# Kernel tuning notes

Hardware: AMD Instinct MI355X
Metric: run time of the kernel (lower is better)

The kernel has to match this reference:

```python
import jax, jax.numpy as jnp
import numpy as np

B, W, F = 32, 128, 64      # batch, window (node feat dim), n_features (nodes)
H, D = 2, 128              # num_heads, out_window_size
NEG_SLOPE = 0.2


def setup_inputs() -> dict:
    key = jax.random.key(0)
    k1, k2, k3, k4, k5 = jax.random.split(key, 5)
    s = 1.0 / np.sqrt(W)
    return {
        "x": jax.random.normal(k1, (B, W, F), dtype=jnp.float32),
        "Wl": jax.random.normal(k2, (W, H * D), dtype=jnp.float32) * s,   # fc_src
        "Wr": jax.random.normal(k3, (W, H * D), dtype=jnp.float32) * s,   # fc_dst
        "attn_a": jax.random.normal(k4, (H, D), dtype=jnp.float32) * s,   # GATv2 attn vector
        "bias": jax.random.normal(k5, (H * D,), dtype=jnp.float32) * 0.01,
    }


def reference(x, Wl, Wr, attn_a, bias):
    """Dense batched GATv2 over a complete graph (with self loops) per batch.

    Matches DGL GATv2Conv (share_weights=False, bias=True, eval mode so
    feat_drop/attn_drop are identity), followed by mean over heads and the
    [B,F,D] -> [B,D,F] transpose of DGLFeatureGAT.forward.
    """
    # node features: x [B, W, F] -> [B, F, W]
    xn = jnp.swapaxes(x, 1, 2)
    el = jnp.einsum('bnw,whd->bnhd', xn, Wl.reshape(W, H, D))  # fc_src(h)
    er = jnp.einsum('bnw,whd->bnhd', xn, Wr.reshape(W, H, D))  # fc_dst(h)
    # edge (src=j -> dst=i): e_ij = a_h . LeakyReLU(el_j + er_i)
    pair = el[:, None, :, :, :] + er[:, :, None, :, :]          # [B, i, j, H, D]
    e = jnp.einsum('bijhd,hd->bhij', jax.nn.leaky_relu(pair, NEG_SLOPE), attn_a)
    # softmax over incoming edges (src j) per dst i
    alpha = jax.nn.softmax(e, axis=-1)                          # [B, H, i, j]
    rst = jnp.einsum('bhij,bjhd->bihd', alpha, el)              # aggregate fc_src feats
    rst = rst + bias.reshape(1, 1, H, D)
    out = rst.mean(axis=2)                                      # mean over heads -> [B, F, D]
    return jnp.swapaxes(out, 1, 2)                              # [B, D, F]
```

## Files before the change

kernel.cpp:

```cpp
#include <hip/hip_runtime.h>
#include <hip/hip_bf16.h>


constexpr int kB = 32, kW = 128, kF = 64, kH = 2, kD = 128, kHD = 256;
constexpr float kNeg = 0.2f;

__device__ __forceinline__ float lrelu(float v) { return fmaxf(v, kNeg * v); }

__global__ __launch_bounds__(512) void gat_proj(
    const float* __restrict__ x, const float* __restrict__ Wl,
    const float* __restrict__ Wr, float* __restrict__ elw,
    float* __restrict__ erw) {
  __shared__ float xw[kW][kF + 4];
  const int b = blockIdx.x >> 3;
  const int c0 = (blockIdx.x & 7) << 5;
  const int t = threadIdx.x;

  const float* xb = x + b * (kW * kF);
#pragma unroll
  for (int k = 0; k < 16; ++k) {
    const int idx = t + (k << 9);
    xw[idx >> 6][idx & 63] = xb[idx];
  }
  __syncthreads();

  const int c = c0 + (t & 31);
  const int n0 = (t >> 5) << 2;
  float accl[4] = {0.f, 0.f, 0.f, 0.f};
  float accr[4] = {0.f, 0.f, 0.f, 0.f};
  const float* wlp = Wl + c;
  const float* wrp = Wr + c;

#pragma unroll 8
  for (int w = 0; w < kW; ++w) {
    const float wl = wlp[w * kHD];
    const float wr = wrp[w * kHD];
    const float4 xa = *(const float4*)&xw[w][n0];
    accl[0] = fmaf(xa.x, wl, accl[0]); accr[0] = fmaf(xa.x, wr, accr[0]);
    accl[1] = fmaf(xa.y, wl, accl[1]); accr[1] = fmaf(xa.y, wr, accr[1]);
    accl[2] = fmaf(xa.z, wl, accl[2]); accr[2] = fmaf(xa.z, wr, accr[2]);
    accl[3] = fmaf(xa.w, wl, accl[3]); accr[3] = fmaf(xa.w, wr, accr[3]);
  }

  const int base = (b * kF + n0) * kHD + c;
#pragma unroll
  for (int k = 0; k < 4; ++k) {
    elw[base + k * kHD] = accl[k];
    erw[base + k * kHD] = accr[k];
  }
}

__global__ __launch_bounds__(512) void gat_attn(
    const float* __restrict__ elw, const float* __restrict__ erw,
    const float* __restrict__ attn_a, const float* __restrict__ bias,
    float* __restrict__ out) {
  __shared__ float el[kH][kF][kD + 4];
  __shared__ float sAT[kH][kF][8];
  __shared__ float pbuf[4][kH][8][kD + 4];

  const int b = blockIdx.x >> 3;
  const int i0 = (blockIdx.x & 7) << 3;
  const int t = threadIdx.x;

  {
    const float* elb = elw + b * (kF * kHD);
#pragma unroll
    for (int k = 0; k < 8; ++k) {
      const int s = t + (k << 9);
      const int h = s >> 11;
      const int n = (s >> 5) & 63;
      const int dv = (s & 31) << 2;
      *(float4*)&el[h][n][dv] = *(const float4*)&elb[n * kHD + h * kD + dv];
    }
  }
  __syncthreads();

  {
    const int q = t & 15;
    const int jh = (t >> 4) & 1;
    const int i = (t >> 5) & 7;
    const int h = t >> 8;
    const int j0 = q + (jh << 5);
    const int j1 = j0 + 16;
    const float* erp = erw + (b * kF + i0 + i) * kHD + h * kD;
    const float* avp = attn_a + h * kD;
    float e0 = 0.f, e1 = 0.f;
#pragma unroll
    for (int dv = 0; dv < kD; dv += 4) {
      const float4 rv = *(const float4*)&erp[dv];
      const float4 a4 = *(const float4*)&avp[dv];
      const float4 p0 = *(const float4*)&el[h][j0][dv];
      const float4 p1 = *(const float4*)&el[h][j1][dv];
      e0 = fmaf(lrelu(p0.x + rv.x), a4.x, e0);
      e0 = fmaf(lrelu(p0.y + rv.y), a4.y, e0);
      e0 = fmaf(lrelu(p0.z + rv.z), a4.z, e0);
      e0 = fmaf(lrelu(p0.w + rv.w), a4.w, e0);
      e1 = fmaf(lrelu(p1.x + rv.x), a4.x, e1);
      e1 = fmaf(lrelu(p1.y + rv.y), a4.y, e1);
      e1 = fmaf(lrelu(p1.z + rv.z), a4.z, e1);
      e1 = fmaf(lrelu(p1.w + rv.w), a4.w, e1);
    }
    float m = fmaxf(e0, e1);
#pragma unroll
    for (int off = 1; off < 32; off <<= 1) m = fmaxf(m, __shfl_xor(m, off));
    const float x0 = __expf(e0 - m);
    const float x1 = __expf(e1 - m);
    float s = x0 + x1;
#pragma unroll
    for (int off = 1; off < 32; off <<= 1) s += __shfl_xor(s, off);
    const float inv = 1.f / s;
    sAT[h][j0][i] = x0 * inv;
    sAT[h][j1][i] = x1 * inv;
  }
  __syncthreads();

  {
    const int dq = t & 31;
    const int ip = (t >> 5) & 1;
    const int jq = (t >> 6) & 3;
    const int h = t >> 8;
    float acc[4][4] = {};
    const int jbase = jq << 4;
#pragma unroll
    for (int jj = 0; jj < 16; ++jj) {
      const int j = jbase + jj;
      const float4 al = *(const float4*)&sAT[h][j][ip << 2];
      const float4 ev = *(const float4*)&el[h][j][dq << 2];
      acc[0][0] = fmaf(al.x, ev.x, acc[0][0]);
      acc[0][1] = fmaf(al.x, ev.y, acc[0][1]);
      acc[0][2] = fmaf(al.x, ev.z, acc[0][2]);
      acc[0][3] = fmaf(al.x, ev.w, acc[0][3]);
      acc[1][0] = fmaf(al.y, ev.x, acc[1][0]);
      acc[1][1] = fmaf(al.y, ev.y, acc[1][1]);
      acc[1][2] = fmaf(al.y, ev.z, acc[1][2]);
      acc[1][3] = fmaf(al.y, ev.w, acc[1][3]);
      acc[2][0] = fmaf(al.z, ev.x, acc[2][0]);
      acc[2][1] = fmaf(al.z, ev.y, acc[2][1]);
      acc[2][2] = fmaf(al.z, ev.z, acc[2][2]);
      acc[2][3] = fmaf(al.z, ev.w, acc[2][3]);
      acc[3][0] = fmaf(al.w, ev.x, acc[3][0]);
      acc[3][1] = fmaf(al.w, ev.y, acc[3][1]);
      acc[3][2] = fmaf(al.w, ev.z, acc[3][2]);
      acc[3][3] = fmaf(al.w, ev.w, acc[3][3]);
    }
#pragma unroll
    for (int ii = 0; ii < 4; ++ii) {
      float4 v;
      v.x = acc[ii][0]; v.y = acc[ii][1]; v.z = acc[ii][2]; v.w = acc[ii][3];
      *(float4*)&pbuf[jq][h][(ip << 2) + ii][dq << 2] = v;
    }
  }
  __syncthreads();

  {
    const int i = t & 7;
    const int d = (t >> 3) << 1;
    float o0 = 0.f, o1 = 0.f;
#pragma unroll
    for (int jq = 0; jq < 4; ++jq) {
#pragma unroll
      for (int h = 0; h < 2; ++h) {
        const float2 v = *(const float2*)&pbuf[jq][h][i][d];
        o0 += v.x;
        o1 += v.y;
      }
    }
    const float b0 = bias[d] + bias[kD + d];
    const float b1 = bias[d + 1] + bias[kD + d + 1];
    float* ob = out + b * (kD * kF) + i0 + i;
    ob[d * kF] = 0.5f * (o0 + b0);
    ob[(d + 1) * kF] = 0.5f * (o1 + b1);
  }
}

extern "C" void kernel_launch(void* const* d_in, const int* in_sizes, int n_in,
                              void* d_out, int out_size, void* d_ws,
                              size_t ws_size, hipStream_t stream) {
  (void)in_sizes; (void)n_in; (void)ws_size; (void)out_size;
  const float* x = (const float*)d_in[0];
  const float* Wl = (const float*)d_in[1];
  const float* Wr = (const float*)d_in[2];
  const float* attn_a = (const float*)d_in[3];
  const float* bias = (const float*)d_in[4];
  float* out = (float*)d_out;

  float* elw = (float*)d_ws;
  float* erw = elw + (size_t)kB * kF * kHD;

  gat_proj<<<dim3(kB * 8), dim3(512), 0, stream>>>(x, Wl, Wr, elw, erw);
  gat_attn<<<dim3(kB * 8), dim3(512), 0, stream>>>(elw, erw, attn_a, bias, out);
}
```

Before: 24.85 us.

## Fuse projection and attention into one kernel, recomputing el per block

Merges the projection and attention kernels into a single kernel. Each block now recomputes the full el projection for its batch in shared memory, plus er for its own 8 destination nodes, instead of round-tripping through a global workspace. This removes one launch and the global write/read of el/er, at the cost of 8x redundant el projection work across the blocks of a batch. Shared memory is reused between the x tile and the partial-sum buffer, and the output store is vectorized as float2 along F.

```diff
diff --git a/kernel.cpp b/kernel.cpp
--- a/kernel.cpp
+++ b/kernel.cpp
@@ -7,89 +7,94 @@
 
 __device__ __forceinline__ float lrelu(float v) { return fmaxf(v, kNeg * v); }
 
-__global__ __launch_bounds__(512) void gat_proj(
+#define XW(w, n) u[(w) * 68 + (n)]
+#define PBUF(jp, h, i, d) u[(((jp) * 2 + (h)) * 8 + (i)) * 132 + (d)]
+
+__global__ __launch_bounds__(512) void gat_fused(
     const float* __restrict__ x, const float* __restrict__ Wl,
-    const float* __restrict__ Wr, float* __restrict__ elw,
-    float* __restrict__ erw) {
-  __shared__ float xw[kW][kF + 4];
+    const float* __restrict__ Wr, const float* __restrict__ attn_a,
+    const float* __restrict__ bias, float* __restrict__ out) {
+  __shared__ float el[kH][kF][kD + 4];
+  __shared__ float er[kH][8][kD + 4];
+  __shared__ float sAT[kH][kF][8];
+  __shared__ float u[8704];
+
   const int b = blockIdx.x >> 3;
-  const int c0 = (blockIdx.x & 7) << 5;
+  const int i0 = (blockIdx.x & 7) << 3;
   const int t = threadIdx.x;
 
   const float* xb = x + b * (kW * kF);
 #pragma unroll
   for (int k = 0; k < 16; ++k) {
     const int idx = t + (k << 9);
-    xw[idx >> 6][idx & 63] = xb[idx];
-  }
-  __syncthreads();
-
-  const int c = c0 + (t & 31);
-  const int n0 = (t >> 5) << 2;
-  float accl[4] = {0.f, 0.f, 0.f, 0.f};
-  float accr[4] = {0.f, 0.f, 0.f, 0.f};
-  const float* wlp = Wl + c;
-  const float* wrp = Wr + c;
-
-#pragma unroll 8
-  for (int w = 0; w < kW; ++w) {
-    const float wl = wlp[w * kHD];
-    const float wr = wrp[w * kHD];
-    const float4 xa = *(const float4*)&xw[w][n0];
-    accl[0] = fmaf(xa.x, wl, accl[0]); accr[0] = fmaf(xa.x, wr, accr[0]);
-    accl[1] = fmaf(xa.y, wl, accl[1]); accr[1] = fmaf(xa.y, wr, accr[1]);
-    accl[2] = fmaf(xa.z, wl, accl[2]); accr[2] = fmaf(xa.z, wr, accr[2]);
-    accl[3] = fmaf(xa.w, wl, accl[3]); accr[3] = fmaf(xa.w, wr, accr[3]);
-  }
-
-  const int base = (b * kF + n0) * kHD + c;
-#pragma unroll
-  for (int k = 0; k < 4; ++k) {
-    elw[base + k * kHD] = accl[k];
-    erw[base + k * kHD] = accr[k];
-  }
-}
-
-__global__ __launch_bounds__(512) void gat_attn(
-    const float* __restrict__ elw, const float* __restrict__ erw,
-    const float* __restrict__ attn_a, const float* __restrict__ bias,
-    float* __restrict__ out) {
-  __shared__ float el[kH][kF][kD + 4];
-  __shared__ float sAT[kH][kF][8];
-  __shared__ float pbuf[4][kH][8][kD + 4];
-
-  const int b = blockIdx.x >> 3;
-  const int i0 = (blockIdx.x & 7) << 3;
-  const int t = threadIdx.x;
-
-  {
-    const float* elb = elw + b * (kF * kHD);
-#pragma unroll
-    for (int k = 0; k < 8; ++k) {
-      const int s = t + (k << 9);
-      const int h = s >> 11;
-      const int n = (s >> 5) & 63;
-      const int dv = (s & 31) << 2;
-      *(float4*)&el[h][n][dv] = *(const float4*)&elb[n * kHD + h * kD + dv];
-    }
+    XW(idx >> 6, idx & 63) = xb[idx];
   }
   __syncthreads();
 
   {
-    const int q = t & 15;
-    const int jh = (t >> 4) & 1;
+    const int dg = t & 31;
+    const int j0 = (t >> 5) << 2;
+    const int c = dg << 2;
+    float a0[4][4] = {};
+    float a1[4][4] = {};
+    const float* w0p = Wl + c;
+    const float* w1p = Wl + kD + c;
+#pragma unroll 4
+    for (int w = 0; w < kW; ++w) {
+      const float4 w0 = *(const float4*)&w0p[w * kHD];
+      const float4 w1 = *(const float4*)&w1p[w * kHD];
+      const float4 xv = *(const float4*)&XW(w, j0);
+      const float xa[4] = {xv.x, xv.y, xv.z, xv.w};
+      const float wa0[4] = {w0.x, w0.y, w0.z, w0.w};
+      const float wa1[4] = {w1.x, w1.y, w1.z, w1.w};
+#pragma unroll
+      for (int jj = 0; jj < 4; ++jj)
+#pragma unroll
+        for (int cc = 0; cc < 4; ++cc) {
+          a0[jj][cc] = fmaf(xa[jj], wa0[cc], a0[jj][cc]);
+          a1[jj][cc] = fmaf(xa[jj], wa1[cc], a1[jj][cc]);
+        }
+    }
+#pragma unroll
+    for (int jj = 0; jj < 4; ++jj) {
+      *(float4*)&el[0][j0 + jj][c] =
+          make_float4(a0[jj][0], a0[jj][1], a0[jj][2], a0[jj][3]);
+      *(float4*)&el[1][j0 + jj][c] =
+          make_float4(a1[jj][0], a1[jj][1], a1[jj][2], a1[jj][3]);
+    }
+  }
+
+  {
+    const int i = t >> 6;
+    const int c = (t & 63) << 2;
+    const int n = i0 + i;
+    float a[4] = {};
+    const float* wrp = Wr + c;
+#pragma unroll 4
+    for (int w = 0; w < kW; ++w) {
+      const float xs = XW(w, n);
+      const float4 w4 = *(const float4*)&wrp[w * kHD];
+      a[0] = fmaf(xs, w4.x, a[0]);
+      a[1] = fmaf(xs, w4.y, a[1]);
+      a[2] = fmaf(xs, w4.z, a[2]);
+      a[3] = fmaf(xs, w4.w, a[3]);
+    }
+    *(float4*)&er[c >> 7][i][c & 127] = make_float4(a[0], a[1], a[2], a[3]);
+  }
+  __syncthreads();
+
+  {
+    const int jl = t & 31;
     const int i = (t >> 5) & 7;
     const int h = t >> 8;
-    const int j0 = q + (jh << 5);
-    const int j1 = j0 + 16;
-    const float* erp = erw + (b * kF + i0 + i) * kHD + h * kD;
+    const int j1 = jl + 32;
     const float* avp = attn_a + h * kD;
     float e0 = 0.f, e1 = 0.f;
 #pragma unroll
     for (int dv = 0; dv < kD; dv += 4) {
-      const float4 rv = *(const float4*)&erp[dv];
       const float4 a4 = *(const float4*)&avp[dv];
-      const float4 p0 = *(const float4*)&el[h][j0][dv];
+      const float4 rv = *(const float4*)&er[h][i][dv];
+      const float4 p0 = *(const float4*)&el[h][jl][dv];
       const float4 p1 = *(const float4*)&el[h][j1][dv];
       e0 = fmaf(lrelu(p0.x + rv.x), a4.x, e0);
       e0 = fmaf(lrelu(p0.y + rv.y), a4.y, e0);
@@ -109,23 +114,24 @@
 #pragma unroll
     for (int off = 1; off < 32; off <<= 1) s += __shfl_xor(s, off);
     const float inv = 1.f / s;
-    sAT[h][j0][i] = x0 * inv;
+    sAT[h][jl][i] = x0 * inv;
     sAT[h][j1][i] = x1 * inv;
   }
   __syncthreads();
 
   {
-    const int dq = t & 31;
-    const int ip = (t >> 5) & 1;
-    const int jq = (t >> 6) & 3;
-    const int h = t >> 8;
+    const int ip = t & 1;
+    const int dg = (t >> 1) & 31;
+    const int h = (t >> 6) & 1;
+    const int jp = t >> 7;
+    const int d0 = dg << 2;
+    const int ib = ip << 2;
     float acc[4][4] = {};
-    const int jbase = jq << 4;
 #pragma unroll
     for (int jj = 0; jj < 16; ++jj) {
-      const int j = jbase + jj;
-      const float4 al = *(const float4*)&sAT[h][j][ip << 2];
-      const float4 ev = *(const float4*)&el[h][j][dq << 2];
+      const int j = (jp << 4) + jj;
+      const float4 al = *(const float4*)&sAT[h][j][ib];
+      const float4 ev = *(const float4*)&el[h][j][d0];
       acc[0][0] = fmaf(al.x, ev.x, acc[0][0]);
       acc[0][1] = fmaf(al.x, ev.y, acc[0][1]);
       acc[0][2] = fmaf(al.x, ev.z, acc[0][2]);
@@ -145,38 +151,36 @@
     }
 #pragma unroll
     for (int ii = 0; ii < 4; ++ii) {
-      float4 v;
-      v.x = acc[ii][0]; v.y = acc[ii][1]; v.z = acc[ii][2]; v.w = acc[ii][3];
-      *(float4*)&pbuf[jq][h][(ip << 2) + ii][dq << 2] = v;
+      *(float4*)&PBUF(jp, h, ib + ii, d0) =
+          make_float4(acc[ii][0], acc[ii][1], acc[ii][2], acc[ii][3]);
     }
   }
   __syncthreads();
 
   {
-    const int i = t & 7;
-    const int d = (t >> 3) << 1;
-    float o0 = 0.f, o1 = 0.f;
+    const int ipr = t & 3;
+    const int d = t >> 2;
+    float s0 = 0.f, s1 = 0.f;
 #pragma unroll
-    for (int jq = 0; jq < 4; ++jq) {
+    for (int jp = 0; jp < 4; ++jp)
 #pragma unroll
       for (int h = 0; h < 2; ++h) {
-        const float2 v = *(const float2*)&pbuf[jq][h][i][d];
-        o0 += v.x;
-        o1 += v.y;
+        const float* p = &PBUF(jp, h, ipr << 1, d);
+        s0 += p[0];
+        s1 += p[132];
       }
-    }
-    const float b0 = bias[d] + bias[kD + d];
-    const float b1 = bias[d + 1] + bias[kD + d + 1];
-    float* ob = out + b * (kD * kF) + i0 + i;
-    ob[d * kF] = 0.5f * (o0 + b0);
-    ob[(d + 1) * kF] = 0.5f * (o1 + b1);
+    const float bs = 0.5f * (bias[d] + bias[kD + d]);
+    float2 v;
+    v.x = 0.5f * s0 + bs;
+    v.y = 0.5f * s1 + bs;
+    *(float2*)&out[b * (kD * kF) + d * kF + i0 + (ipr << 1)] = v;
   }
 }
 
 extern "C" void kernel_launch(void* const* d_in, const int* in_sizes, int n_in,
                               void* d_out, int out_size, void* d_ws,
                               size_t ws_size, hipStream_t stream) {
-  (void)in_sizes; (void)n_in; (void)ws_size; (void)out_size;
+  (void)in_sizes; (void)n_in; (void)d_ws; (void)ws_size; (void)out_size;
   const float* x = (const float*)d_in[0];
   const float* Wl = (const float*)d_in[1];
   const float* Wr = (const float*)d_in[2];
@@ -184,9 +188,6 @@
   const float* bias = (const float*)d_in[4];
   float* out = (float*)d_out;
 
-  float* elw = (float*)d_ws;
-  float* erw = elw + (size_t)kB * kF * kHD;
-
-  gat_proj<<<dim3(kB * 8), dim3(512), 0, stream>>>(x, Wl, Wr, elw, erw);
-  gat_attn<<<dim3(kB * 8), dim3(512), 0, stream>>>(elw, erw, attn_a, bias, out);
+  gat_fused<<<dim3(kB * 8), dim3(512), 0, stream>>>(x, Wl, Wr, attn_a, bias,
+                                                    out);
 }
```

After: 32.85 us. 1.32x slower.

## Double threads per block and split per-thread work in GAT kernels

Applied to the files above, without the earlier changes.

Both kernels move from 512 to 1024 threads per block, and each thread does half the work. In the projection each thread now computes 2 nodes instead of 4. In the attention score phase the D reduction is split across two thread halves and combined with a cross-lane shuffle, and each thread also uses two accumulators. The aggregation now handles 2 rows per thread, and the final reduce writes one output per thread. The goal is more parallelism and latency hiding with only 256 blocks on the device, at the cost of extra shuffles and heavier per-block register and LDS pressure.

```diff
diff --git a/kernel.cpp b/kernel.cpp
--- a/kernel.cpp
+++ b/kernel.cpp
@@ -7,7 +7,7 @@
 
 __device__ __forceinline__ float lrelu(float v) { return fmaxf(v, kNeg * v); }
 
-__global__ __launch_bounds__(512) void gat_proj(
+__global__ __launch_bounds__(1024) void gat_proj(
     const float* __restrict__ x, const float* __restrict__ Wl,
     const float* __restrict__ Wr, float* __restrict__ elw,
     float* __restrict__ erw) {
@@ -18,16 +18,15 @@
 
   const float* xb = x + b * (kW * kF);
 #pragma unroll
-  for (int k = 0; k < 16; ++k) {
-    const int idx = t + (k << 9);
+  for (int k = 0; k < 8; ++k) {
+    const int idx = t + (k << 10);
     xw[idx >> 6][idx & 63] = xb[idx];
   }
   __syncthreads();
 
   const int c = c0 + (t & 31);
-  const int n0 = (t >> 5) << 2;
-  float accl[4] = {0.f, 0.f, 0.f, 0.f};
-  float accr[4] = {0.f, 0.f, 0.f, 0.f};
+  const int n0 = (t >> 5) << 1;
+  float l0 = 0.f, l1 = 0.f, r0 = 0.f, r1 = 0.f;
   const float* wlp = Wl + c;
   const float* wrp = Wr + c;
 
@@ -35,22 +34,21 @@
   for (int w = 0; w < kW; ++w) {
     const float wl = wlp[w * kHD];
     const float wr = wrp[w * kHD];
-    const float4 xa = *(const float4*)&xw[w][n0];
-    accl[0] = fmaf(xa.x, wl, accl[0]); accr[0] = fmaf(xa.x, wr, accr[0]);
-    accl[1] = fmaf(xa.y, wl, accl[1]); accr[1] = fmaf(xa.y, wr, accr[1]);
-    accl[2] = fmaf(xa.z, wl, accl[2]); accr[2] = fmaf(xa.z, wr, accr[2]);
-    accl[3] = fmaf(xa.w, wl, accl[3]); accr[3] = fmaf(xa.w, wr, accr[3]);
+    const float2 xa = *(const float2*)&xw[w][n0];
+    l0 = fmaf(xa.x, wl, l0);
+    r0 = fmaf(xa.x, wr, r0);
+    l1 = fmaf(xa.y, wl, l1);
+    r1 = fmaf(xa.y, wr, r1);
   }
 
   const int base = (b * kF + n0) * kHD + c;
-#pragma unroll
-  for (int k = 0; k < 4; ++k) {
-    elw[base + k * kHD] = accl[k];
-    erw[base + k * kHD] = accr[k];
-  }
+  elw[base] = l0;
+  elw[base + kHD] = l1;
+  erw[base] = r0;
+  erw[base + kHD] = r1;
 }
 
-__global__ __launch_bounds__(512) void gat_attn(
+__global__ __launch_bounds__(1024) void gat_attn(
     const float* __restrict__ elw, const float* __restrict__ erw,
     const float* __restrict__ attn_a, const float* __restrict__ bias,
     float* __restrict__ out) {
@@ -65,8 +63,8 @@
   {
     const float* elb = elw + b * (kF * kHD);
 #pragma unroll
-    for (int k = 0; k < 8; ++k) {
-      const int s = t + (k << 9);
+    for (int k = 0; k < 4; ++k) {
+      const int s = t + (k << 10);
       const int h = s >> 11;
       const int n = (s >> 5) & 63;
       const int dv = (s & 31) << 2;
@@ -78,28 +76,46 @@
   {
     const int q = t & 15;
     const int jh = (t >> 4) & 1;
-    const int i = (t >> 5) & 7;
-    const int h = t >> 8;
+    const int dh = (t >> 5) & 1;
+    const int i = (t >> 6) & 7;
+    const int h = t >> 9;
     const int j0 = q + (jh << 5);
     const int j1 = j0 + 16;
     const float* erp = erw + (b * kF + i0 + i) * kHD + h * kD;
     const float* avp = attn_a + h * kD;
-    float e0 = 0.f, e1 = 0.f;
+    const int dvb = dh << 6;
+    float e0a = 0.f, e0b = 0.f, e1a = 0.f, e1b = 0.f;
 #pragma unroll
-    for (int dv = 0; dv < kD; dv += 4) {
+    for (int k = 0; k < 16; ++k) {
+      const int dv = dvb + (k << 2);
+      const float4 a4 = *(const float4*)&avp[dv];
       const float4 rv = *(const float4*)&erp[dv];
-      const float4 a4 = *(const float4*)&avp[dv];
       const float4 p0 = *(const float4*)&el[h][j0][dv];
       const float4 p1 = *(const float4*)&el[h][j1][dv];
-      e0 = fmaf(lrelu(p0.x + rv.x), a4.x, e0);
-      e0 = fmaf(lrelu(p0.y + rv.y), a4.y, e0);
-      e0 = fmaf(lrelu(p0.z + rv.z), a4.z, e0);
-      e0 = fmaf(lrelu(p0.w + rv.w), a4.w, e0);
-      e1 = fmaf(lrelu(p1.x + rv.x), a4.x, e1);
-      e1 = fmaf(lrelu(p1.y + rv.y), a4.y, e1);
-      e1 = fmaf(lrelu(p1.z + rv.z), a4.z, e1);
-      e1 = fmaf(lrelu(p1.w + rv.w), a4.w, e1);
+      if (k & 1) {
+        e0b = fmaf(lrelu(p0.x + rv.x), a4.x, e0b);
+        e0b = fmaf(lrelu(p0.y + rv.y), a4.y, e0b);
+        e0b = fmaf(lrelu(p0.z + rv.z), a4.z, e0b);
+        e0b = fmaf(lrelu(p0.w + rv.w), a4.w, e0b);
+        e1b = fmaf(lrelu(p1.x + rv.x), a4.x, e1b);
+        e1b = fmaf(lrelu(p1.y + rv.y), a4.y, e1b);
+        e1b = fmaf(lrelu(p1.z + rv.z), a4.z, e1b);
+        e1b = fmaf(lrelu(p1.w + rv.w), a4.w, e1b);
+      } else {
+        e0a = fmaf(lrelu(p0.x + rv.x), a4.x, e0a);
+        e0a = fmaf(lrelu(p0.y + rv.y), a4.y, e0a);
+        e0a = fmaf(lrelu(p0.z + rv.z), a4.z, e0a);
+        e0a = fmaf(lrelu(p0.w + rv.w), a4.w, e0a);
+        e1a = fmaf(lrelu(p1.x + rv.x), a4.x, e1a);
+        e1a = fmaf(lrelu(p1.y + rv.y), a4.y, e1a);
+        e1a = fmaf(lrelu(p1.z + rv.z), a4.z, e1a);
+        e1a = fmaf(lrelu(p1.w + rv.w), a4.w, e1a);
+      }
     }
+    float e0 = e0a + e0b;
+    float e1 = e1a + e1b;
+    e0 += __shfl_xor(e0, 32);
+    e1 += __shfl_xor(e1, 32);
     float m = fmaxf(e0, e1);
 #pragma unroll
     for (int off = 1; off < 32; off <<= 1) m = fmaxf(m, __shfl_xor(m, off));
@@ -116,16 +132,17 @@
 
   {
     const int dq = t & 31;
-    const int ip = (t >> 5) & 1;
-    const int jq = (t >> 6) & 3;
-    const int h = t >> 8;
-    float acc[4][4] = {};
-    const int jbase = jq << 4;
+    const int jq = (t >> 5) & 3;
+    const int isel = (t >> 7) & 3;
+    const int h = t >> 9;
+    const int d0 = dq << 2;
+    const int i2 = isel << 1;
+    float acc[2][4] = {};
 #pragma unroll
     for (int jj = 0; jj < 16; ++jj) {
-      const int j = jbase + jj;
-      const float4 al = *(const float4*)&sAT[h][j][ip << 2];
-      const float4 ev = *(const float4*)&el[h][j][dq << 2];
+      const int j = (jq << 4) + jj;
+      const float2 al = *(const float2*)&sAT[h][j][i2];
+      const float4 ev = *(const float4*)&el[h][j][d0];
       acc[0][0] = fmaf(al.x, ev.x, acc[0][0]);
       acc[0][1] = fmaf(al.x, ev.y, acc[0][1]);
       acc[0][2] = fmaf(al.x, ev.z, acc[0][2]);
@@ -134,42 +151,24 @@
       acc[1][1] = fmaf(al.y, ev.y, acc[1][1]);
       acc[1][2] = fmaf(al.y, ev.z, acc[1][2]);
       acc[1][3] = fmaf(al.y, ev.w, acc[1][3]);
-      acc[2][0] = fmaf(al.z, ev.x, acc[2][0]);
-      acc[2][1] = fmaf(al.z, ev.y, acc[2][1]);
-      acc[2][2] = fmaf(al.z, ev.z, acc[2][2]);
-      acc[2][3] = fmaf(al.z, ev.w, acc[2][3]);
-      acc[3][0] = fmaf(al.w, ev.x, acc[3][0]);
-      acc[3][1] = fmaf(al.w, ev.y, acc[3][1]);
-      acc[3][2] = fmaf(al.w, ev.z, acc[3][2]);
-      acc[3][3] = fmaf(al.w, ev.w, acc[3][3]);
     }
-#pragma unroll
-    for (int ii = 0; ii < 4; ++ii) {
-      float4 v;
-      v.x = acc[ii][0]; v.y = acc[ii][1]; v.z = acc[ii][2]; v.w = acc[ii][3];
-      *(float4*)&pbuf[jq][h][(ip << 2) + ii][dq << 2] = v;
-    }
+    *(float4*)&pbuf[jq][h][i2][d0] =
+        make_float4(acc[0][0], acc[0][1], acc[0][2], acc[0][3]);
+    *(float4*)&pbuf[jq][h][i2 + 1][d0] =
+        make_float4(acc[1][0], acc[1][1], acc[1][2], acc[1][3]);
   }
   __syncthreads();
 
   {
     const int i = t & 7;
-    const int d = (t >> 3) << 1;
-    float o0 = 0.f, o1 = 0.f;
+    const int d = t >> 3;
+    float s = 0.f;
 #pragma unroll
-    for (int jq = 0; jq < 4; ++jq) {
+    for (int jq = 0; jq < 4; ++jq)
 #pragma unroll
-      for (int h = 0; h < 2; ++h) {
-        const float2 v = *(const float2*)&pbuf[jq][h][i][d];
-        o0 += v.x;
-        o1 += v.y;
-      }
-    }
-    const float b0 = bias[d] + bias[kD + d];
-    const float b1 = bias[d + 1] + bias[kD + d + 1];
-    float* ob = out + b * (kD * kF) + i0 + i;
-    ob[d * kF] = 0.5f * (o0 + b0);
-    ob[(d + 1) * kF] = 0.5f * (o1 + b1);
+      for (int h = 0; h < 2; ++h) s += pbuf[jq][h][i][d];
+    const float bs = 0.5f * (bias[d] + bias[kD + d]);
+    out[b * (kD * kF) + d * kF + i0 + i] = 0.5f * s + bs;
   }
 }
 
@@ -187,6 +186,7 @@
   float* elw = (float*)d_ws;
   float* erw = elw + (size_t)kB * kF * kHD;
 
-  gat_proj<<<dim3(kB * 8), dim3(512), 0, stream>>>(x, Wl, Wr, elw, erw);
-  gat_attn<<<dim3(kB * 8), dim3(512), 0, stream>>>(elw, erw, attn_a, bias, out);
+  gat_proj<<<dim3(kB * 8), dim3(1024), 0, stream>>>(x, Wl, Wr, elw, erw);
+  gat_attn<<<dim3(kB * 8), dim3(1024), 0, stream>>>(elw, erw, attn_a, bias,
+                                                    out);
 }
```

Result: slower. 32.31 us (+30.0%).
